# Kernel optimization log

Measured on AMD Instinct MI355X. Metric: run time of the kernel, lower is better.

The kernel has to match this reference:

```python
import jax, jax.numpy as jnp
import numpy as np


def _graph_conv(feat_src, e_src, e_dst, n_src, n_dst, W, b):
    # DGL GraphConv, norm='both', bipartite block; feat_src: [N_src, A, C, H]
    ones_e = jnp.ones(e_src.shape[0], dtype=feat_src.dtype)
    out_deg = jax.ops.segment_sum(ones_e, e_src, num_segments=n_src)
    in_deg = jax.ops.segment_sum(ones_e, e_dst, num_segments=n_dst)
    norm_src = jnp.clip(out_deg, 1.0) ** -0.5
    norm_dst = jnp.clip(in_deg, 1.0) ** -0.5
    feat = feat_src * norm_src[:, None, None, None]
    # in_feats == out_feats -> DGL multiplies by W before aggregation
    feat = jnp.einsum('nach,ho->naco', feat, W)
    msgs = feat[e_src]                                   # gather  [E, A, C, H]
    agg = jax.ops.segment_sum(msgs, e_dst, num_segments=n_dst)  # scatter-add
    return agg * norm_dst[:, None, None, None] + b


def setup_inputs() -> dict:
    key = jax.random.key(0)
    ks = jax.random.split(key, 8)
    H = 128
    N_SRC0, N_DST0, N_DST1 = 50000, 20000, 4096
    E0, E1 = 320000, 65536
    return {
        'in_feat': jax.random.normal(ks[0], (2, H, 2, N_SRC0), dtype=jnp.float32),
        'W': jax.random.normal(ks[1], (H, H), dtype=jnp.float32) / np.sqrt(H),
        'b': jnp.zeros((H,), dtype=jnp.float32),
        'e0_src': jax.random.randint(ks[2], (E0,), 0, N_SRC0, dtype=jnp.int32),
        'e0_dst': jax.random.randint(ks[3], (E0,), 0, N_DST0, dtype=jnp.int32),
        'e1_src': jax.random.randint(ks[4], (E1,), 0, N_DST0, dtype=jnp.int32),
        'e1_dst': jax.random.randint(ks[5], (E1,), 0, N_DST1, dtype=jnp.int32),
        'n_dst0': N_DST0,
        'n_dst1': N_DST1,
    }


def reference(in_feat, W, b, e0_src, e0_dst, e1_src, e1_dst, n_dst0, n_dst1):
    # [A, H, C, N] -> [N, A, C, H]
    x = jnp.transpose(in_feat, (3, 0, 2, 1))
    n_src0 = x.shape[0]
    h = _graph_conv(x, e0_src, e0_dst, n_src0, n_dst0, W, b)
    h = jax.nn.relu(h)
    h = _graph_conv(h, e1_src, e1_dst, n_dst0, n_dst1, W, b)
    h = jax.nn.relu(h)
    # [N_dst1, A, C, H] -> [A, H, C, N_dst1]
    out = jnp.transpose(h, (1, 3, 2, 0))
    return jax.nn.relu(out)
```

## Files before the change

kernel.cpp:

```cpp
#include <hip/hip_runtime.h>
#include <math.h>

#define H128 128
#define NF 512
typedef unsigned short u16;
typedef __attribute__((ext_vector_type(8))) short short8;
typedef __attribute__((ext_vector_type(4))) float floatx4;

__device__ inline u16 f2bf(float f) {
  union { float f; unsigned u; } x; x.f = f;
  unsigned r = x.u + 0x7FFFu + ((x.u >> 16) & 1u);
  return (u16)(r >> 16);
}
__device__ inline void addbf8(float* a, uint4 u) {
  a[0] += __uint_as_float(u.x << 16);
  a[1] += __uint_as_float(u.x & 0xFFFF0000u);
  a[2] += __uint_as_float(u.y << 16);
  a[3] += __uint_as_float(u.y & 0xFFFF0000u);
  a[4] += __uint_as_float(u.z << 16);
  a[5] += __uint_as_float(u.z & 0xFFFF0000u);
  a[6] += __uint_as_float(u.w << 16);
  a[7] += __uint_as_float(u.w & 0xFFFF0000u);
}

__global__ void k_count2(const int* __restrict__ e0s, const int* __restrict__ e0d,
                         const int* __restrict__ e1s, const int* __restrict__ e1d,
                         int E0, int E1,
                         int* __restrict__ c_s0, int* __restrict__ c_d0,
                         int* __restrict__ c_s1, int* __restrict__ c_d1) {
  int i = blockIdx.x * 256 + threadIdx.x;
  if (i < E0) {
    atomicAdd(&c_s0[e0s[i]], 1);
    atomicAdd(&c_d0[e0d[i]], 1);
    return;
  }
  i -= E0;
  if (i < E1) {
    atomicAdd(&c_s1[e1s[i]], 1);
    atomicAdd(&c_d1[e1d[i]], 1);
  }
}

__global__ __launch_bounds__(1024) void k_prep(
    const int* __restrict__ cnt, int NCNT, float* __restrict__ normf,
    const int* __restrict__ degA, int nA, int* __restrict__ offA, int* __restrict__ curA,
    const int* __restrict__ degB, int nB, int* __restrict__ offB, int* __restrict__ curB,
    const float* __restrict__ W, uint4* __restrict__ wfrag) {
  __shared__ int wsum[16];
  const int b = blockIdx.x;
  const int tid = threadIdx.x;
  if (b < 2) {
    const int* deg = b ? degB : degA;
    int n = b ? nB : nA;
    int* off = b ? offB : offA;
    int* cur = b ? curB : curA;
    const int lane = tid & 63;
    const int wv = tid >> 6;
    const int per = (n + 1023) >> 10;
    const int base = tid * per;
    int cntk = n - base;
    if (cntk < 0) cntk = 0;
    if (cntk > per) cntk = per;
    int sum = 0;
    for (int i = 0; i < cntk; ++i) sum += deg[base + i];
    int x = sum;
    #pragma unroll
    for (int d2 = 1; d2 < 64; d2 <<= 1) {
      int y = __shfl_up(x, (unsigned)d2, 64);
      if (lane >= d2) x += y;
    }
    if (lane == 63) wsum[wv] = x;
    __syncthreads();
    if (wv == 0 && lane < 16) {
      int w = wsum[lane];
      #pragma unroll
      for (int d2 = 1; d2 < 16; d2 <<= 1) {
        int y = __shfl_up(w, (unsigned)d2, 64);
        if (lane >= d2) w += y;
      }
      wsum[lane] = w;
    }
    __syncthreads();
    int tbase = x - sum + (wv ? wsum[wv - 1] : 0);
    int running = tbase;
    for (int i = 0; i < cntk; ++i) {
      off[base + i] = running;
      cur[base + i] = running;
      running += deg[base + i];
    }
    if (tid == 1023) off[n] = wsum[15];
    return;
  }
  if (b < 4) {
    int t = (b - 2) * 1024 + tid;
    if (t < 2048) {
      int lane = t & 63;
      int pair = t >> 6;
      int ct = pair >> 2, kc = pair & 3;
      int quad = lane >> 4, r = lane & 15;
      const float* src = W + (size_t)(kc * 32 + quad * 8) * 128 + ct * 16 + r;
      union { u16 v[8]; uint4 u; } pk;
      #pragma unroll
      for (int j = 0; j < 8; ++j) pk.v[j] = f2bf(src[(size_t)j * 128]);
      wfrag[t] = pk.u;
    }
    return;
  }
  int i = (b - 4) * 1024 + tid;
  if (i < NCNT) {
    int d = cnt[i];
    float dv = (d < 1) ? 1.0f : (float)d;
    normf[i] = 1.0f / sqrtf(dv);
  }
}

__global__ __launch_bounds__(512) void k_tin_scatter(
    const float* __restrict__ in, const float* __restrict__ norm,
    u16* __restrict__ xp, int N, int SB,
    const int* __restrict__ e0s, const int* __restrict__ e0d,
    const int* __restrict__ e1s, const int* __restrict__ e1d,
    int E0, int E1,
    int* __restrict__ cur0, int* __restrict__ csr0,
    int* __restrict__ cur1, int* __restrict__ csr1) {
  __shared__ float tile[256 * 32];
  const int bid = blockIdx.x;
  const int tid = threadIdx.x;
  if (bid < SB) {
    #pragma unroll
    for (int k = 0; k < 4; ++k) {
      int i = (bid * 4 + k) * 512 + tid;
      if (i < E0) {
        int p = atomicAdd(&cur0[e0d[i]], 1);
        csr0[p] = e0s[i];
      } else {
        i -= E0;
        if (i < E1) {
          int p = atomicAdd(&cur1[e1d[i]], 1);
          csr1[p] = e1s[i];
        }
      }
    }
    return;
  }
  const int tb = bid - SB;
  const int hc = tb & 3;
  const int ac = (tb >> 2) & 3;
  const int ti = tb >> 4;
  const int n0 = ti << 8;
  const int h0 = hc << 5;
  const int a = ac >> 1, c = ac & 1;
  const float* base = in + ((size_t)a * 256 + (size_t)h0 * 2 + c) * (size_t)N;
  const int lane = tid & 63;
  const int w = tid >> 6;
  const int gnl = n0 + (lane << 2);
  float4 v[4];
  #pragma unroll
  for (int i = 0; i < 4; ++i) {
    const int hl = i * 8 + w;
    v[i] = make_float4(0.f, 0.f, 0.f, 0.f);
    if (gnl < N) v[i] = *(const float4*)(base + (size_t)hl * 2 * N + gnl);
  }
  #pragma unroll
  for (int i = 0; i < 4; ++i) {
    const int hl = i * 8 + w;
    float vv[4] = {v[i].x, v[i].y, v[i].z, v[i].w};
    #pragma unroll
    for (int j = 0; j < 4; ++j) {
      const int nl = (lane << 2) + j;
      const int cs = (hl + nl + (nl >> 5)) & 31;
      tile[nl * 32 + cs] = vv[j];
    }
  }
  __syncthreads();
  #pragma unroll
  for (int i = 0; i < 4; ++i) {
    const int nl = i * 64 + (tid >> 3);
    const int gn = n0 + nl;
    if (gn < N) {
      const int hq = tid & 7;
      const float s = norm[gn];
      const int rb = nl * 32;
      const int ofs = nl + (nl >> 5);
      float f0 = tile[rb + ((4 * hq + 0 + ofs) & 31)];
      float f1 = tile[rb + ((4 * hq + 1 + ofs) & 31)];
      float f2 = tile[rb + ((4 * hq + 2 + ofs) & 31)];
      float f3 = tile[rb + ((4 * hq + 3 + ofs) & 31)];
      ushort4 o;
      o.x = f2bf(f0 * s); o.y = f2bf(f1 * s);
      o.z = f2bf(f2 * s); o.w = f2bf(f3 * s);
      *(ushort4*)(xp + (size_t)gn * NF + ac * H128 + h0 + hq * 4) = o;
    }
  }
}

template <int MODE>
__global__ __launch_bounds__(256) void k_agg_gemm(
    const u16* __restrict__ xp, const int* __restrict__ csr,
    const int* __restrict__ off, const float* __restrict__ norm_dst,
    const uint4* __restrict__ wfrag, const float* __restrict__ bias,
    const float* __restrict__ scale, void* __restrict__ outv, int Nout) {
  __shared__ uint4 wb[2048];
  __shared__ u16 atile[16][520];
  const int tid = threadIdx.x;
  #pragma unroll
  for (int i = 0; i < 8; ++i) wb[i * 256 + tid] = wfrag[i * 256 + tid];
  const int wave = tid >> 6;
  const int lane = tid & 63;
  const int d0 = blockIdx.x << 4;
  const uint4* xpl = (const uint4*)xp + lane;
  #pragma unroll
  for (int i = 0; i < 4; ++i) {
    const int m = wave * 4 + i;
    const int d = d0 + m;
    const int s = off[d], e = off[d + 1];
    float acc[8];
    #pragma unroll
    for (int k = 0; k < 8; ++k) acc[k] = 0.f;
    int j = s;
    for (; j + 8 <= e; j += 8) {
      uint4 u[8];
      #pragma unroll
      for (int k = 0; k < 8; ++k) u[k] = xpl[(size_t)csr[j + k] * 64];
      #pragma unroll
      for (int k = 0; k < 8; ++k) addbf8(acc, u[k]);
    }
    for (; j < e; ++j) addbf8(acc, xpl[(size_t)csr[j] * 64]);
    float nd = norm_dst[d];
    union { u16 v[8]; uint4 u; } pk;
    #pragma unroll
    for (int k = 0; k < 8; ++k) pk.v[k] = f2bf(acc[k] * nd);
    *(uint4*)&atile[m][lane * 8] = pk.u;
  }
  __syncthreads();
  const int quad = lane >> 4;
  const int r = lane & 15;
  short8 a[4];
  #pragma unroll
  for (int kc = 0; kc < 4; ++kc)
    a[kc] = *(const short8*)&atile[r][wave * 128 + kc * 32 + quad * 8];
  floatx4 acc[8];
  #pragma unroll
  for (int ct = 0; ct < 8; ++ct) acc[ct] = (floatx4){0.f, 0.f, 0.f, 0.f};
  #pragma unroll
  for (int kc = 0; kc < 4; ++kc) {
    #pragma unroll
    for (int ct = 0; ct < 8; ++ct) {
      short8 b = *(const short8*)&wb[(ct * 4 + kc) * 64 + lane];
      acc[ct] = __builtin_amdgcn_mfma_f32_16x16x32_bf16(a[kc], b, acc[ct], 0, 0, 0);
    }
  }
  if (MODE == 0) {
    float sc[4];
    #pragma unroll
    for (int reg = 0; reg < 4; ++reg) sc[reg] = scale[d0 + quad * 4 + reg];
    #pragma unroll
    for (int ct = 0; ct < 8; ++ct) {
      float bcol = bias[ct * 16 + r];
      #pragma unroll
      for (int reg = 0; reg < 4; ++reg) {
        float v = acc[ct][reg] + bcol;
        v = (v > 0.f ? v : 0.f) * sc[reg];
        ((u16*)outv)[(size_t)(d0 + quad * 4 + reg) * NF + wave * H128 + ct * 16 + r] = f2bf(v);
      }
    }
  } else {
    const int aa = wave >> 1, cc = wave & 1;
    #pragma unroll
    for (int ct = 0; ct < 8; ++ct) {
      float bcol = bias[ct * 16 + r];
      float4 o;
      float v0 = acc[ct][0] + bcol; o.x = v0 > 0.f ? v0 : 0.f;
      float v1 = acc[ct][1] + bcol; o.y = v1 > 0.f ? v1 : 0.f;
      float v2 = acc[ct][2] + bcol; o.z = v2 > 0.f ? v2 : 0.f;
      float v3 = acc[ct][3] + bcol; o.w = v3 > 0.f ? v3 : 0.f;
      float* dst = (float*)outv +
          ((size_t)aa * 256 + (size_t)(ct * 16 + r) * 2 + cc) * (size_t)Nout +
          d0 + quad * 4;
      *(float4*)dst = o;
    }
  }
}

extern "C" void kernel_launch(void* const* d_in, const int* in_sizes, int n_in,
                              void* d_out, int out_size, void* d_ws, size_t ws_size,
                              hipStream_t stream) {
  const float* in_feat = (const float*)d_in[0];
  const float* W       = (const float*)d_in[1];
  const float* bias    = (const float*)d_in[2];
  const int* e0_src    = (const int*)d_in[3];
  const int* e0_dst    = (const int*)d_in[4];
  const int* e1_src    = (const int*)d_in[5];
  const int* e1_dst    = (const int*)d_in[6];
  const int N_DST0 = 20000;
  const int N_DST1 = 4096;
  const int N_SRC0 = in_sizes[0] / NF;
  const int E0 = in_sizes[3];
  const int E1 = in_sizes[5];

  u16* xp = (u16*)d_ws;
  u16* h0 = xp + (size_t)N_SRC0 * NF;
  int* ibase    = (int*)(h0 + (size_t)N_DST0 * NF);
  int* cnt_src0 = ibase;
  int* cnt_dst0 = cnt_src0 + N_SRC0;
  int* cnt_src1 = cnt_dst0 + N_DST0;
  int* cnt_dst1 = cnt_src1 + N_DST0;
  int* off0 = cnt_dst1 + N_DST1;
  int* cur0 = off0 + N_DST0 + 1;
  int* csr0 = cur0 + N_DST0;
  int* off1 = csr0 + E0;
  int* cur1 = off1 + N_DST1 + 1;
  int* csr1 = cur1 + N_DST1;
  uint4* wfrag = (uint4*)(((uintptr_t)(csr1 + E1) + 15) & ~(uintptr_t)15);
  float* normf = (float*)(wfrag + 2048);
  float* normf_src0 = normf;
  float* normf_dst0 = normf_src0 + N_SRC0;
  float* normf_src1 = normf_dst0 + N_DST0;
  float* normf_dst1 = normf_src1 + N_DST0;

  const int NCNT = N_SRC0 + N_DST0 + N_DST0 + N_DST1;
  hipMemsetAsync(cnt_src0, 0, (size_t)NCNT * sizeof(int), stream);

  k_count2<<<(E0 + E1 + 255) / 256, 256, 0, stream>>>(
      e0_src, e0_dst, e1_src, e1_dst, E0, E1, cnt_src0, cnt_dst0, cnt_src1, cnt_dst1);

  k_prep<<<4 + (NCNT + 1023) / 1024, 1024, 0, stream>>>(
      cnt_src0, NCNT, normf,
      cnt_dst0, N_DST0, off0, cur0,
      cnt_dst1, N_DST1, off1, cur1,
      W, wfrag);

  const int SB = (E0 + E1 + 2047) / 2048;
  const int ntiles = (N_SRC0 + 255) / 256;
  const int TB = ntiles * 16;
  k_tin_scatter<<<SB + TB, 512, 0, stream>>>(
      in_feat, normf_src0, xp, N_SRC0, SB,
      e0_src, e0_dst, e1_src, e1_dst, E0, E1,
      cur0, csr0, cur1, csr1);

  k_agg_gemm<0><<<N_DST0 / 16, 256, 0, stream>>>(
      xp, csr0, off0, normf_dst0, wfrag, bias, normf_src1, (void*)h0, 0);

  k_agg_gemm<1><<<N_DST1 / 16, 256, 0, stream>>>(
      h0, csr1, off1, normf_dst1, wfrag, bias, nullptr, d_out, N_DST1);
}
```

Measured before the change: 336.5 us.

## Restructure transpose tiles to full rows, deepen gather unroll, read W fragments from global

The transpose kernel now gives each block 64 nodes covering all 512 features, and stages bf16 values in shared memory so each node row goes out as full contiguous 16-byte stores. The previous layout wrote 8-byte pieces spread across rows. The aggregation kernel raises the gather unroll depth to 12 or 16 and adds a 4-wide remainder loop, putting more loads in flight per destination. It also stops staging W fragments in shared memory and has the MFMA loop read them straight from global or cache, which cuts LDS use and may raise occupancy. The costs are higher register pressure from the deeper unroll and repeated global reads of W.

```diff
diff --git a/kernel.cpp b/kernel.cpp
--- a/kernel.cpp
+++ b/kernel.cpp
@@ -122,7 +122,7 @@
     int E0, int E1,
     int* __restrict__ cur0, int* __restrict__ csr0,
     int* __restrict__ cur1, int* __restrict__ csr1) {
-  __shared__ float tile[256 * 32];
+  __shared__ u16 tile[64][520];
   const int bid = blockIdx.x;
   const int tid = threadIdx.x;
   if (bid < SB) {
@@ -143,52 +143,55 @@
     return;
   }
   const int tb = bid - SB;
-  const int hc = tb & 3;
-  const int ac = (tb >> 2) & 3;
-  const int ti = tb >> 4;
-  const int n0 = ti << 8;
-  const int h0 = hc << 5;
-  const int a = ac >> 1, c = ac & 1;
-  const float* base = in + ((size_t)a * 256 + (size_t)h0 * 2 + c) * (size_t)N;
+  const int n0 = tb << 6;
+  const int t = tid & 15;
+  const int fq_loc = tid >> 4;
+  const int gn4 = n0 + (t << 2);
+  float4 s4 = make_float4(0.f, 0.f, 0.f, 0.f);
+  if (gn4 < N) s4 = *(const float4*)(norm + gn4);
+  float sA[4] = {s4.x, s4.y, s4.z, s4.w};
+  float4 v[4][4];
+  #pragma unroll
+  for (int i = 0; i < 4; ++i) {
+    const int a = i >> 1, c = i & 1;
+    const float* base = in + ((size_t)a * 256 + (size_t)(fq_loc << 2) * 2 + c) * (size_t)N;
+    #pragma unroll
+    for (int k = 0; k < 4; ++k) {
+      v[i][k] = make_float4(0.f, 0.f, 0.f, 0.f);
+      if (gn4 < N) v[i][k] = *(const float4*)(base + (size_t)(2 * k) * N + gn4);
+    }
+  }
+  #pragma unroll
+  for (int i = 0; i < 4; ++i) {
+    const int fq = i * 32 + fq_loc;
+    float va[4][4];
+    #pragma unroll
+    for (int k = 0; k < 4; ++k) {
+      va[k][0] = v[i][k].x; va[k][1] = v[i][k].y;
+      va[k][2] = v[i][k].z; va[k][3] = v[i][k].w;
+    }
+    #pragma unroll
+    for (int j = 0; j < 4; ++j) {
+      const int n = (t << 2) + j;
+      const float sj = sA[j];
+      ushort4 o;
+      o.x = f2bf(va[0][j] * sj);
+      o.y = f2bf(va[1][j] * sj);
+      o.z = f2bf(va[2][j] * sj);
+      o.w = f2bf(va[3][j] * sj);
+      *(ushort4*)&tile[n][fq << 2] = o;
+    }
+  }
+  __syncthreads();
+  const int w = tid >> 6;
   const int lane = tid & 63;
-  const int w = tid >> 6;
-  const int gnl = n0 + (lane << 2);
-  float4 v[4];
-  #pragma unroll
-  for (int i = 0; i < 4; ++i) {
-    const int hl = i * 8 + w;
-    v[i] = make_float4(0.f, 0.f, 0.f, 0.f);
-    if (gnl < N) v[i] = *(const float4*)(base + (size_t)hl * 2 * N + gnl);
-  }
-  #pragma unroll
-  for (int i = 0; i < 4; ++i) {
-    const int hl = i * 8 + w;
-    float vv[4] = {v[i].x, v[i].y, v[i].z, v[i].w};
-    #pragma unroll
-    for (int j = 0; j < 4; ++j) {
-      const int nl = (lane << 2) + j;
-      const int cs = (hl + nl + (nl >> 5)) & 31;
-      tile[nl * 32 + cs] = vv[j];
-    }
-  }
-  __syncthreads();
-  #pragma unroll
-  for (int i = 0; i < 4; ++i) {
-    const int nl = i * 64 + (tid >> 3);
-    const int gn = n0 + nl;
+  #pragma unroll
+  for (int m = 0; m < 8; ++m) {
+    const int n = (m << 3) + w;
+    const int gn = n0 + n;
     if (gn < N) {
-      const int hq = tid & 7;
-      const float s = norm[gn];
-      const int rb = nl * 32;
-      const int ofs = nl + (nl >> 5);
-      float f0 = tile[rb + ((4 * hq + 0 + ofs) & 31)];
-      float f1 = tile[rb + ((4 * hq + 1 + ofs) & 31)];
-      float f2 = tile[rb + ((4 * hq + 2 + ofs) & 31)];
-      float f3 = tile[rb + ((4 * hq + 3 + ofs) & 31)];
-      ushort4 o;
-      o.x = f2bf(f0 * s); o.y = f2bf(f1 * s);
-      o.z = f2bf(f2 * s); o.w = f2bf(f3 * s);
-      *(ushort4*)(xp + (size_t)gn * NF + ac * H128 + h0 + hq * 4) = o;
+      uint4 q = *(const uint4*)&tile[n][lane << 3];
+      *(uint4*)(xp + (size_t)gn * NF + (lane << 3)) = q;
     }
   }
 }
@@ -199,11 +202,9 @@
     const int* __restrict__ off, const float* __restrict__ norm_dst,
     const uint4* __restrict__ wfrag, const float* __restrict__ bias,
     const float* __restrict__ scale, void* __restrict__ outv, int Nout) {
-  __shared__ uint4 wb[2048];
   __shared__ u16 atile[16][520];
+  constexpr int DEPTH = (MODE == 0) ? 12 : 16;
   const int tid = threadIdx.x;
-  #pragma unroll
-  for (int i = 0; i < 8; ++i) wb[i * 256 + tid] = wfrag[i * 256 + tid];
   const int wave = tid >> 6;
   const int lane = tid & 63;
   const int d0 = blockIdx.x << 4;
@@ -217,12 +218,19 @@
     #pragma unroll
     for (int k = 0; k < 8; ++k) acc[k] = 0.f;
     int j = s;
-    for (; j + 8 <= e; j += 8) {
-      uint4 u[8];
-      #pragma unroll
-      for (int k = 0; k < 8; ++k) u[k] = xpl[(size_t)csr[j + k] * 64];
-      #pragma unroll
-      for (int k = 0; k < 8; ++k) addbf8(acc, u[k]);
+    for (; j + DEPTH <= e; j += DEPTH) {
+      uint4 u[DEPTH];
+      #pragma unroll
+      for (int k = 0; k < DEPTH; ++k) u[k] = xpl[(size_t)csr[j + k] * 64];
+      #pragma unroll
+      for (int k = 0; k < DEPTH; ++k) addbf8(acc, u[k]);
+    }
+    for (; j + 4 <= e; j += 4) {
+      uint4 u[4];
+      #pragma unroll
+      for (int k = 0; k < 4; ++k) u[k] = xpl[(size_t)csr[j + k] * 64];
+      #pragma unroll
+      for (int k = 0; k < 4; ++k) addbf8(acc, u[k]);
     }
     for (; j < e; ++j) addbf8(acc, xpl[(size_t)csr[j] * 64]);
     float nd = norm_dst[d];
@@ -245,7 +253,7 @@
   for (int kc = 0; kc < 4; ++kc) {
     #pragma unroll
     for (int ct = 0; ct < 8; ++ct) {
-      short8 b = *(const short8*)&wb[(ct * 4 + kc) * 64 + lane];
+      short8 b = *(const short8*)&wfrag[(ct * 4 + kc) * 64 + lane];
       acc[ct] = __builtin_amdgcn_mfma_f32_16x16x32_bf16(a[kc], b, acc[ct], 0, 0, 0);
     }
   }
@@ -330,8 +338,7 @@
       W, wfrag);
 
   const int SB = (E0 + E1 + 2047) / 2048;
-  const int ntiles = (N_SRC0 + 255) / 256;
-  const int TB = ntiles * 16;
+  const int TB = (N_SRC0 + 63) / 64;
   k_tin_scatter<<<SB + TB, 512, 0, stream>>>(
       in_feat, normf_src0, xp, N_SRC0, SB,
       e0_src, e0_dst, e1_src, e1_dst, E0, E1,
```

Result: faster. 329.4 us (-2.1%).
